# Kernel tuning notes

Hardware: AMD Instinct MI355X
Metric: run time of the kernel (lower is better)

## Reference

```python
import jax, jax.numpy as jnp
import numpy as np

HEADS = 8


def setup_inputs() -> dict:
    key = jax.random.key(0)
    ks = jax.random.split(key, 7)
    b, t, e, h = 4, 2048, 128, HEADS
    x = jax.random.normal(ks[0], (b, t, e), dtype=jnp.float32)
    mask = jax.random.randint(ks[1], (1, t, t), 0, 2, dtype=jnp.int32)
    Wq = jax.random.normal(ks[2], (e, e * h), dtype=jnp.float32) / np.sqrt(e)
    Wk = jax.random.normal(ks[3], (e, e * h), dtype=jnp.float32) / np.sqrt(e)
    Wv = jax.random.normal(ks[4], (e, e * h), dtype=jnp.float32) / np.sqrt(e)
    Wu = jax.random.normal(ks[5], (e * h, e), dtype=jnp.float32) / np.sqrt(e * h)
    bu = jax.random.normal(ks[6], (e,), dtype=jnp.float32) * 0.01
    return {"x": x, "mask": mask, "Wq": Wq, "Wk": Wk, "Wv": Wv, "Wu": Wu, "bu": bu}


def reference(x, mask, Wq, Wk, Wv, Wu, bu):
    b, t, e = x.shape
    h = HEADS
    scale = e ** (-0.25)  # original scales q and k each by e**(1/4)
    # project and split heads: (b, t, h, e) -> (b, h, t, e)
    q = (x @ Wq).reshape(b, t, h, e).transpose(0, 2, 1, 3) * scale
    k = (x @ Wk).reshape(b, t, h, e).transpose(0, 2, 1, 3) * scale
    v = (x @ Wv).reshape(b, t, h, e).transpose(0, 2, 1, 3)
    dot = jnp.einsum('bhqe,bhke->bhqk', q, k)  # (b, h, t, t)
    # causal mask: strictly-upper triangle set to -inf (mask_diagonal=False -> offset=1)
    causal = jnp.triu(jnp.ones((t, t), dtype=bool), k=1)
    dot = jnp.where(causal, jnp.float32(-np.inf), dot)
    # external mask: positions where mask == 0 set to -1e9 (broadcast over b*h)
    dot = jnp.where((mask == 0)[:, None, :, :], jnp.float32(-1e9), dot)
    att = jax.nn.softmax(dot, axis=-1)
    out = jnp.einsum('bhqk,bhke->bhqe', att, v)
    out = out.transpose(0, 2, 1, 3).reshape(b, t, h * e)
    return out @ Wu + bu
```

## Files before the change

### kernel.cpp

```cpp
#include <hip/hip_runtime.h>
#include <hip/hip_bf16.h>

typedef unsigned short u16;
typedef unsigned int u32;
typedef __attribute__((ext_vector_type(8))) short bf16x8;
typedef __attribute__((ext_vector_type(4))) float f32x4;
typedef __attribute__((ext_vector_type(8))) unsigned short u16x8;
typedef __attribute__((ext_vector_type(2))) unsigned int u32x2;

#define T_ 2048
#define H_ 8
#define BH_ 32
#define M_ 8192
#define SCALE_QK 0.29730177875068026f
#define LOG2E 1.4426950408889634f

__device__ __forceinline__ u16 f2bf(float f) {
  union { __hip_bfloat16 h; u16 u; } cv; cv.h = __float2bfloat16(f); return cv.u;
}
__device__ __forceinline__ float bf2f(u16 u) {
  union { u16 u; __hip_bfloat16 h; } cv; cv.u = u; return __bfloat162float(cv.h);
}


__global__ __launch_bounds__(256)
void prep_kernel(const float* __restrict__ x, const float* __restrict__ Wq,
                 const float* __restrict__ Wk, const float* __restrict__ Wv,
                 const float* __restrict__ Wu,
                 u16* __restrict__ xb, u16* __restrict__ WT, u16* __restrict__ WuT)
{
  int i = blockIdx.x * 256 + threadIdx.x;
  if (i < M_ * 128) { xb[i] = f2bf(x[i]); return; }
  int j = i - M_ * 128;
  if (j < 3072 * 128) {
    int n = j >> 7, k = j & 127;
    float w;
    if (n < 1024)      w = Wq[k * 1024 + n] * (SCALE_QK * LOG2E);
    else if (n < 2048) w = Wk[k * 1024 + (n - 1024)] * SCALE_QK;
    else               w = Wv[k * 1024 + (n - 2048)];
    WT[j] = f2bf(w);
    return;
  }
  int u = j - 3072 * 128;
  if (u < 128 * 1024) {
    int n = u >> 10, k = u & 1023;
    WuT[u] = f2bf(Wu[k * 128 + n]);
  }
}

__global__ __launch_bounds__(256)
void maskprep_kernel(const int* __restrict__ mask, u32* __restrict__ mbits,
                     u32* __restrict__ deglist, u32* __restrict__ degcount,
                     float* __restrict__ cnt0inv)
{
  int wave = threadIdx.x >> 6, lane = threadIdx.x & 63;
  int q = blockIdx.x * 4 + wave;
  const int* row = mask + (long)q * 2048;
  unsigned long long anyvis = 0ull;
  int cnt1 = 0;
  for (int it = 0; it < 32; ++it) {
    int k = it * 64 + lane;
    unsigned long long bal = __ballot(row[k] != 0);
    if (lane == 0) {
      mbits[q * 64 + it * 2]     = (u32)bal;
      mbits[q * 64 + it * 2 + 1] = (u32)(bal >> 32);
    }
    cnt1 += __popcll(bal);
    int lim = q - it * 64;
    if (lim >= 63)      anyvis |= bal;
    else if (lim >= 0)  anyvis |= (bal & ((2ull << lim) - 1ull));
  }
  if (lane == 0) {
    int c0 = 2048 - cnt1;
    cnt0inv[q] = (c0 > 0) ? 1.0f / (float)c0 : 0.0f;
    if (anyvis == 0ull) {
      u32 slot = atomicAdd(degcount, 1u);
      deglist[slot] = (u32)q;
    }
  }
}

__global__ __launch_bounds__(256)
void qkv_kernel(const u16* __restrict__ xb, const u16* __restrict__ WT,
                u16* __restrict__ Qb, u16* __restrict__ Kimg, u16* __restrict__ Vimg)
{
  __shared__ __align__(16) u16 As[128 * 128];
  __shared__ __align__(16) u16 Bs[128 * 128];
  const int tid = threadIdx.x;
  const int n0 = blockIdx.x * 128;
  const int m0 = blockIdx.y * 128;
#pragma unroll
  for (int i = 0; i < 8; ++i) {
    int c = tid + 256 * i;
    int row = c >> 4, d0 = (c & 15) * 8;
    int soff = row * 128 + ((((d0 >> 3)) ^ (row & 15)) << 3);
    *(u16x8*)(&As[soff]) = *(const u16x8*)(&xb[(m0 + row) * 128 + d0]);
    *(u16x8*)(&Bs[soff]) = *(const u16x8*)(&WT[(n0 + row) * 128 + d0]);
  }
  __syncthreads();
  const int wave = tid >> 6, lane = tid & 63;
  const int lr = lane & 15, lg = lane >> 4;
  const int wm = (wave >> 1) * 64, wn = (wave & 1) * 64;
  f32x4 acc[4][4];
#pragma unroll
  for (int a = 0; a < 4; ++a)
#pragma unroll
    for (int b = 0; b < 4; ++b) acc[a][b] = (f32x4){0.f, 0.f, 0.f, 0.f};
#pragma unroll
  for (int ks = 0; ks < 4; ++ks) {
    bf16x8 af[4], bf[4];
#pragma unroll
    for (int mt = 0; mt < 4; ++mt) {
      int row = wm + mt * 16 + lr, chunk = lg + ks * 4;
      af[mt] = *(const bf16x8*)(&As[row * 128 + ((chunk ^ (row & 15)) << 3)]);
    }
#pragma unroll
    for (int nt = 0; nt < 4; ++nt) {
      int row = wn + nt * 16 + lr, chunk = lg + ks * 4;
      bf[nt] = *(const bf16x8*)(&Bs[row * 128 + ((chunk ^ (row & 15)) << 3)]);
    }
#pragma unroll
    for (int mt = 0; mt < 4; ++mt)
#pragma unroll
      for (int nt = 0; nt < 4; ++nt)
        acc[mt][nt] = __builtin_amdgcn_mfma_f32_16x16x32_bf16(af[mt], bf[nt], acc[mt][nt], 0, 0, 0);
  }
  const int mat = n0 >> 10;
  const int hh = (n0 & 1023) >> 7;
  const int bb = m0 >> 11;
  const long bhb = (long)(bb * H_ + hh);
  __syncthreads();
  if (mat != 2) {
#pragma unroll
    for (int mt = 0; mt < 4; ++mt)
#pragma unroll
      for (int nt = 0; nt < 4; ++nt)
#pragma unroll
        for (int r = 0; r < 4; ++r) {
          int tl = wm + mt * 16 + lg * 4 + r;
          int d  = wn + nt * 16 + lr;
          As[tl * 128 + ((((d >> 3)) ^ (tl & 15)) << 3) + (d & 7)] = f2bf(acc[mt][nt][r]);
        }
    __syncthreads();
    if (mat == 0) {
#pragma unroll
      for (int i = 0; i < 8; ++i) {
        int c = tid + 256 * i;
        int row = c >> 4, d0 = (c & 15) * 8;
        u16x8 v = *(const u16x8*)(&As[row * 128 + ((((d0 >> 3)) ^ (row & 15)) << 3)]);
        *(u16x8*)(&Qb[(bhb * T_ + ((m0 + row) & 2047)) * 128 + d0]) = v;
      }
    } else {
#pragma unroll
      for (int i = 0; i < 8; ++i) {
        int c = tid + 256 * i;
        int row = c >> 4, d0 = (c & 15) * 8;
        u16x8 v = *(const u16x8*)(&As[row * 128 + ((((d0 >> 3)) ^ (row & 15)) << 3)]);
        int t = (m0 + row) & 2047;
        int kt = t >> 6, kr = t & 63;
        *(u16x8*)(&Kimg[(bhb * 32 + kt) * 8192 + kr * 128 + ((((d0 >> 3)) ^ (kr & 15)) << 3)]) = v;
      }
    }
  } else {
    u16* TT = As;
#pragma unroll
    for (int mt = 0; mt < 4; ++mt)
#pragma unroll
      for (int nt = 0; nt < 4; ++nt)
#pragma unroll
        for (int r = 0; r < 4; ++r) {
          int tl = wm + mt * 16 + lg * 4 + r;
          int d  = wn + nt * 16 + lr;
          TT[d * 128 + ((((tl >> 3)) ^ (d & 15)) << 3) + (tl & 7)] = f2bf(acc[mt][nt][r]);
        }
    __syncthreads();
    const int tg0 = m0 & 2047;
#pragma unroll
    for (int i = 0; i < 8; ++i) {
      int c = tid + 256 * i;
      int d = c >> 4, t0 = (c & 15) * 8;
      u16x8 v = *(const u16x8*)(&TT[d * 128 + ((((t0 >> 3)) ^ (d & 15)) << 3)]);
      int tg = tg0 + t0;
      int kt = tg >> 6, kk = tg & 63;
      *(u16x8*)(&Vimg[(bhb * 32 + kt) * 8192 + d * 64 + (((kk >> 3) ^ (d & 7)) << 3)]) = v;
    }
  }
}

__global__ __launch_bounds__(256, 3)
void flash_kernel(const u16* __restrict__ Qb, const u16* __restrict__ Kimg,
                  const u16* __restrict__ Vimg, const u32* __restrict__ mbits,
                  u16* __restrict__ Ob)
{
  __shared__ __align__(16) u16 Ks[64 * 128];
  __shared__ __align__(16) u16 VTs[128 * 64];
  __shared__ __align__(16) u16 Ps[4][16 * 64];
  const int tid = threadIdx.x;
  const int g = blockIdx.x >> 5;
  const int a_ = g & 7, quad = g >> 3;
  const int qt = (quad == 0) ? (31 - a_) : (quad == 1) ? (8 + a_)
               : (quad == 2) ? (23 - a_) : a_;
  const int bh = blockIdx.x & 31;
  const int q0 = qt * 64;
  const int wave = tid >> 6, lane = tid & 63;
  const int lr = lane & 15, lg = lane >> 4;
  const long base = (long)bh * T_ * 128;
  const long iblk = (long)bh * 32;
  const int ldsoff = wave * 2048 + lane * 8;
  const int qrl = wave * 16 + lr;
  const int swz = (lr & 7) << 1;

  bf16x8 qf[4];
  {
    const u16* qrow = Qb + base + (long)(q0 + qrl) * 128;
#pragma unroll
    for (int ks = 0; ks < 4; ++ks)
      qf[ks] = *(const bf16x8*)(&qrow[lg * 8 + ks * 32]);
  }
  f32x4 acc[8];
#pragma unroll
  for (int i = 0; i < 8; ++i) acc[i] = (f32x4){0.f, 0.f, 0.f, 0.f};
  float mrun = -__builtin_inff(), lrun = 0.f;

  u16x8 kreg[4], vreg[4];
  {
    const u16* ks0 = Kimg + iblk * 8192 + ldsoff;
    const u16* vs0 = Vimg + iblk * 8192 + ldsoff;
#pragma unroll
    for (int i = 0; i < 4; ++i) {
      kreg[i] = *(const u16x8*)(ks0 + i * 512);
      vreg[i] = *(const u16x8*)(vs0 + i * 512);
    }
  }

  for (int kt = 0; kt <= qt; ++kt) {
    __syncthreads();
#pragma unroll
    for (int i = 0; i < 4; ++i) {
      *(u16x8*)(&Ks[ldsoff + i * 512]) = kreg[i];
      *(u16x8*)(&VTs[ldsoff + i * 512]) = vreg[i];
    }
    __syncthreads();
    if (kt < qt) {
      const u16* ksn = Kimg + (iblk + kt + 1) * 8192 + ldsoff;
      const u16* vsn = Vimg + (iblk + kt + 1) * 8192 + ldsoff;
#pragma unroll
      for (int i = 0; i < 4; ++i) {
        kreg[i] = *(const u16x8*)(ksn + i * 512);
        vreg[i] = *(const u16x8*)(vsn + i * 512);
      }
    }
    u32 mw0, mw1;
    {
      const u32* mp = &mbits[(q0 + qrl) * 64 + kt * 2];
      mw0 = mp[0]; mw1 = mp[1];
    }

    f32x4 s[4];
    __builtin_amdgcn_s_setprio(1);
#pragma unroll
    for (int ft = 0; ft < 4; ++ft) {
      f32x4 sa = (f32x4){0.f, 0.f, 0.f, 0.f};
#pragma unroll
      for (int ks = 0; ks < 4; ++ks) {
        int kr = ft * 16 + lr, chunk = lg + ks * 4;
        bf16x8 kf = *(const bf16x8*)(&Ks[kr * 128 + ((chunk ^ (kr & 15)) << 3)]);
        sa = __builtin_amdgcn_mfma_f32_16x16x32_bf16(kf, qf[ks], sa, 0, 0, 0);
      }
      s[ft] = sa;
    }
    __builtin_amdgcn_s_setprio(0);
    const bool diag = (kt == qt);
#pragma unroll
    for (int ft = 0; ft < 4; ++ft) {
      u32 w = (ft & 2) ? mw1 : mw0;
      int kbase = ft * 16 + lg * 4;
      int sh = ((ft & 1) << 4) + lg * 4;
#pragma unroll
      for (int r = 0; r < 4; ++r) {
        bool vis = (w >> (sh + r)) & 1u;
        if (diag && (kbase + r) > qrl) vis = false;
        if (!vis) s[ft][r] = -__builtin_inff();
      }
    }
    float t0 = fmaxf(fmaxf(s[0][0], s[0][1]), fmaxf(s[0][2], s[0][3]));
    float t1 = fmaxf(fmaxf(s[1][0], s[1][1]), fmaxf(s[1][2], s[1][3]));
    float t2 = fmaxf(fmaxf(s[2][0], s[2][1]), fmaxf(s[2][2], s[2][3]));
    float t3 = fmaxf(fmaxf(s[3][0], s[3][1]), fmaxf(s[3][2], s[3][3]));
    float tm = fmaxf(fmaxf(t0, t1), fmaxf(t2, t3));
    tm = fmaxf(tm, __shfl_xor(tm, 16));
    tm = fmaxf(tm, __shfl_xor(tm, 32));
    float mnew = fmaxf(mrun, tm);
    float msafe = (mnew == -__builtin_inff()) ? 0.f : mnew;
    float fac = __builtin_amdgcn_exp2f(mrun - msafe);
    const bool grew = (mnew != mrun);
    mrun = mnew;
    float rs = 0.f;
#pragma unroll
    for (int ft = 0; ft < 4; ++ft) {
      float p0 = __builtin_amdgcn_exp2f(s[ft][0] - msafe);
      float p1 = __builtin_amdgcn_exp2f(s[ft][1] - msafe);
      float p2 = __builtin_amdgcn_exp2f(s[ft][2] - msafe);
      float p3 = __builtin_amdgcn_exp2f(s[ft][3] - msafe);
      s[ft][0] = p0; s[ft][1] = p1; s[ft][2] = p2; s[ft][3] = p3;
      rs += (p0 + p1) + (p2 + p3);
    }
    rs += __shfl_xor(rs, 16);
    rs += __shfl_xor(rs, 32);
    lrun = lrun * fac + rs;
    if (__any(grew)) {
#pragma unroll
      for (int nt = 0; nt < 8; ++nt)
#pragma unroll
        for (int r = 0; r < 4; ++r) acc[nt][r] *= fac;
    }
#pragma unroll
    for (int ft = 0; ft < 4; ++ft) {
      u16 h0 = f2bf(s[ft][0]), h1 = f2bf(s[ft][1]);
      u16 h2 = f2bf(s[ft][2]), h3 = f2bf(s[ft][3]);
      u32x2 pw; pw[0] = (u32)h0 | ((u32)h1 << 16); pw[1] = (u32)h2 | ((u32)h3 << 16);
      int ch4 = (ft * 4 + lg) ^ swz;
      *(u32x2*)(&Ps[wave][lr * 64 + ch4 * 4]) = pw;
    }
    bf16x8 pa[2];
#pragma unroll
    for (int s2 = 0; s2 < 2; ++s2) {
      int ch4b = (s2 * 8 + lg * 2) ^ swz;
      pa[s2] = *(const bf16x8*)(&Ps[wave][lr * 64 + ch4b * 4]);
    }
    __builtin_amdgcn_s_setprio(1);
#pragma unroll
    for (int nt = 0; nt < 8; ++nt)
#pragma unroll
      for (int s2 = 0; s2 < 2; ++s2) {
        int d = nt * 16 + lr, chunk = lg + s2 * 4;
        bf16x8 vf = *(const bf16x8*)(&VTs[d * 64 + ((chunk ^ (d & 7)) << 3)]);
        acc[nt] = __builtin_amdgcn_mfma_f32_16x16x32_bf16(vf, pa[s2], acc[nt], 0, 0, 0);
      }
    __builtin_amdgcn_s_setprio(0);
  }
  const float inv = (lrun > 0.f) ? 1.f / lrun : 0.f;
  const long orow = base + (long)(q0 + qrl) * 128;
#pragma unroll
  for (int nt = 0; nt < 8; ++nt) {
    u16 h0 = f2bf(acc[nt][0] * inv), h1 = f2bf(acc[nt][1] * inv);
    u16 h2 = f2bf(acc[nt][2] * inv), h3 = f2bf(acc[nt][3] * inv);
    u32x2 ow; ow[0] = (u32)h0 | ((u32)h1 << 16); ow[1] = (u32)h2 | ((u32)h3 << 16);
    *(u32x2*)(&Ob[orow + nt * 16 + lg * 4]) = ow;
  }
}

__global__ __launch_bounds__(256)
void fixup_partial_kernel(const u32* __restrict__ deglist, const u32* __restrict__ degcount,
                          const u32* __restrict__ mbits, const u16* __restrict__ Vimg,
                          float* __restrict__ partial)
{
  const int slot = blockIdx.z;
  const u32 cnt = *degcount;
  if (slot >= (int)cnt) return;
  const int ksec = blockIdx.x, bh = blockIdx.y;
  const int q = (int)deglist[slot];
  const int t = threadIdx.x;
  const int d = t & 127, kc = t >> 7;
  const u16* vb = Vimg + ((long)bh * 32 + ksec) * 8192 + d * 64;
  const u32 w0 = mbits[q * 64 + ksec * 2];
  const u32 w1 = mbits[q * 64 + ksec * 2 + 1];
  float a = 0.f;
#pragma unroll
  for (int i = 0; i < 4; ++i) {
    int c = kc * 4 + i;
    u32 bits = ((kc == 0) ? (w0 >> (c * 8)) : (w1 >> ((c - 4) * 8))) & 0xffu;
    u16x8 v = *(const u16x8*)(&vb[(c ^ (d & 7)) << 3]);
#pragma unroll
    for (int j = 0; j < 8; ++j)
      a += ((bits >> j) & 1u) ? 0.f : bf2f(v[j]);
  }
  __shared__ float tmp[2][128];
  tmp[kc][d] = a;
  __syncthreads();
  if (t < 128)
    partial[(((long)slot * BH_ + bh) * 128 + d) * 32 + ksec] = tmp[0][d] + tmp[1][d];
}

__global__ __launch_bounds__(128)
void fixup_combine_kernel(const u32* __restrict__ deglist, const u32* __restrict__ degcount,
                          const float* __restrict__ cnt0inv, const float* __restrict__ partial,
                          u16* __restrict__ Ob)
{
  const int slot = blockIdx.x;
  const u32 cnt = *degcount;
  if (slot >= (int)cnt) return;
  const int bh = blockIdx.y;
  const int q = (int)deglist[slot];
  const int d = threadIdx.x;
  const float* p = partial + (((long)slot * BH_ + bh) * 128 + d) * 32;
  float s = 0.f;
#pragma unroll
  for (int i = 0; i < 8; ++i) {
    f32x4 v = *(const f32x4*)(&p[i * 4]);
    s += (v[0] + v[1]) + (v[2] + v[3]);
  }
  Ob[((long)bh * T_ + q) * 128 + d] = f2bf(s * cnt0inv[q]);
}

__global__ __launch_bounds__(256)
void fixup_slow_kernel(const u32* __restrict__ deglist, const u32* __restrict__ degcount,
                       const float* __restrict__ cnt0inv, const u32* __restrict__ mbits,
                       const u16* __restrict__ Vimg, u16* __restrict__ Ob)
{
  const u32 cnt = *degcount;
  const int bh = blockIdx.y;
  const int d = threadIdx.x & 127, half = threadIdx.x >> 7;
  __shared__ float tmp[2][128];
  const u16* vb = Vimg + (long)bh * 32 * 8192;
  for (u32 idx = 8 + blockIdx.x; idx < cnt; idx += gridDim.x) {
    const int q = (int)deglist[idx];
    const float inv = cnt0inv[q];
    float a = 0.f;
#pragma unroll 16
    for (int i = 0; i < 128; ++i) {
      int k0 = half * 1024 + i * 8;
      u32 w = mbits[q * 64 + (k0 >> 5)];
      u32 bits = (w >> (k0 & 31)) & 0xffu;
      int kt = k0 >> 6, kk = k0 & 63;
      u16x8 v = *(const u16x8*)(&vb[(long)kt * 8192 + d * 64 + (((kk >> 3) ^ (d & 7)) << 3)]);
#pragma unroll
      for (int j = 0; j < 8; ++j)
        a += ((bits >> j) & 1u) ? 0.f : bf2f(v[j]);
    }
    tmp[half][d] = a;
    __syncthreads();
    if (half == 0)
      Ob[((long)bh * T_ + q) * 128 + d] = f2bf((tmp[0][d] + tmp[1][d]) * inv);
    __syncthreads();
  }
}

__global__ __launch_bounds__(256)
void outproj_kernel(const u16* __restrict__ Ob, const u16* __restrict__ WuT,
                    const float* __restrict__ bu, float* __restrict__ out)
{
  __shared__ __align__(16) u16 As[32 * 128];
  __shared__ __align__(16) u16 Bs[128 * 128];
  const int tid = threadIdx.x;
  const int m0 = blockIdx.x * 32;
  const int wave = tid >> 6, lane = tid & 63;
  const int lr = lane & 15, lg = lane >> 4;
  f32x4 acc[2][2];
#pragma unroll
  for (int a = 0; a < 2; ++a)
#pragma unroll
    for (int b = 0; b < 2; ++b) acc[a][b] = (f32x4){0.f, 0.f, 0.f, 0.f};
  for (int kc = 0; kc < 8; ++kc) {
    __syncthreads();
#pragma unroll
    for (int i = 0; i < 2; ++i) {
      int c = tid + 256 * i;
      int row = c >> 4, d0 = (c & 15) * 8;
      int m = m0 + row, bb = m >> 11, t = m & 2047;
      *(u16x8*)(&As[row * 128 + ((((d0 >> 3)) ^ (row & 15)) << 3)]) =
          *(const u16x8*)(&Ob[((long)(bb * H_ + kc) * T_ + t) * 128 + d0]);
    }
#pragma unroll
    for (int i = 0; i < 8; ++i) {
      int c = tid + 256 * i;
      int row = c >> 4, d0 = (c & 15) * 8;
      *(u16x8*)(&Bs[row * 128 + ((((d0 >> 3)) ^ (row & 15)) << 3)]) =
          *(const u16x8*)(&WuT[row * 1024 + kc * 128 + d0]);
    }
    __syncthreads();
#pragma unroll
    for (int ks = 0; ks < 4; ++ks) {
      bf16x8 af[2], bf2[2];
#pragma unroll
      for (int mt = 0; mt < 2; ++mt) {
        int row = mt * 16 + lr, chunk = lg + ks * 4;
        af[mt] = *(const bf16x8*)(&As[row * 128 + ((chunk ^ (row & 15)) << 3)]);
      }
#pragma unroll
      for (int nt = 0; nt < 2; ++nt) {
        int row = wave * 32 + nt * 16 + lr, chunk = lg + ks * 4;
        bf2[nt] = *(const bf16x8*)(&Bs[row * 128 + ((chunk ^ (row & 15)) << 3)]);
      }
#pragma unroll
      for (int mt = 0; mt < 2; ++mt)
#pragma unroll
        for (int nt = 0; nt < 2; ++nt)
          acc[mt][nt] = __builtin_amdgcn_mfma_f32_16x16x32_bf16(af[mt], bf2[nt], acc[mt][nt], 0, 0, 0);
    }
  }
#pragma unroll
  for (int mt = 0; mt < 2; ++mt)
#pragma unroll
    for (int nt = 0; nt < 2; ++nt) {
      int n = wave * 32 + nt * 16 + lr;
      float bias = bu[n];
#pragma unroll
      for (int r = 0; r < 4; ++r) {
        int m = m0 + mt * 16 + lg * 4 + r;
        out[(long)m * 128 + n] = acc[mt][nt][r] + bias;
      }
    }
}

extern "C" void kernel_launch(void* const* d_in, const int* in_sizes, int n_in,
                              void* d_out, int out_size, void* d_ws, size_t ws_size,
                              hipStream_t stream)
{
  (void)in_sizes; (void)n_in; (void)out_size; (void)ws_size;
  const float* x   = (const float*)d_in[0];
  const int*   msk = (const int*)d_in[1];
  const float* Wq  = (const float*)d_in[2];
  const float* Wk  = (const float*)d_in[3];
  const float* Wv  = (const float*)d_in[4];
  const float* Wu  = (const float*)d_in[5];
  const float* bu  = (const float*)d_in[6];
  float* out = (float*)d_out;

  u16* Qb   = (u16*)d_ws;
  u16* Kimg = Qb + (size_t)BH_ * T_ * 128;
  u16* Vimg = Kimg + (size_t)BH_ * T_ * 128;
  u16* Obf  = Vimg + (size_t)BH_ * T_ * 128;
  u16* xb   = Obf + (size_t)BH_ * T_ * 128;
  u16* WT   = xb + (size_t)M_ * 128;
  u16* WuT  = WT + (size_t)3072 * 128;
  u32* mbits   = (u32*)(WuT + (size_t)128 * 1024);
  u32* deglist = mbits + (size_t)2048 * 64;
  u32* degcount = deglist + 2048;
  float* cnt0inv = (float*)(degcount + 1);
  float* partial = (float*)Qb;

  hipMemsetAsync(degcount, 0, sizeof(u32), stream);
  prep_kernel<<<6144, 256, 0, stream>>>(x, Wq, Wk, Wv, Wu, xb, WT, WuT);
  maskprep_kernel<<<512, 256, 0, stream>>>(msk, mbits, deglist, degcount, cnt0inv);
  qkv_kernel<<<dim3(24, 64), 256, 0, stream>>>(xb, WT, Qb, Kimg, Vimg);
  flash_kernel<<<1024, 256, 0, stream>>>(Qb, Kimg, Vimg, mbits, Obf);
  fixup_partial_kernel<<<dim3(32, 32, 8), 256, 0, stream>>>(deglist, degcount, mbits, Vimg, partial);
  fixup_combine_kernel<<<dim3(8, 32), 128, 0, stream>>>(deglist, degcount, cnt0inv, partial, Obf);
  fixup_slow_kernel<<<dim3(32, 32), 256, 0, stream>>>(deglist, degcount, cnt0inv, mbits, Vimg, Obf);
  outproj_kernel<<<256, 256, 0, stream>>>(Obf, WuT, bu, out);
}
```

Measured before the change: 134.1 us.

## Load V fragments directly from global memory and add lazy softmax rescaling

Drops the V tile from shared memory. Each wave now loads its V MFMA operands straight from the pre-swizzled global V image into registers, split into two halves so the loads overlap with the softmax and QK work. This removes V LDS writes and reads and shrinks LDS usage, which could raise occupancy. It also adds a lazy rescale that skips updating the running max and rescaling the accumulator when no lane's max grows by more than 8 (log2 units). This trades extra global/L2 traffic, since every wave re-reads V, and more register pressure for less LDS traffic and less rescaling work.

```diff
diff --git a/kernel.cpp b/kernel.cpp
--- a/kernel.cpp
+++ b/kernel.cpp
@@ -193,7 +193,6 @@
                   u16* __restrict__ Ob)
 {
   __shared__ __align__(16) u16 Ks[64 * 128];
-  __shared__ __align__(16) u16 VTs[128 * 64];
   __shared__ __align__(16) u16 Ps[4][16 * 64];
   const int tid = threadIdx.x;
   const int g = blockIdx.x >> 5;
@@ -222,34 +221,40 @@
   for (int i = 0; i < 8; ++i) acc[i] = (f32x4){0.f, 0.f, 0.f, 0.f};
   float mrun = -__builtin_inff(), lrun = 0.f;
 
-  u16x8 kreg[4], vreg[4];
+  int voff[8][2];
+#pragma unroll
+  for (int nt = 0; nt < 8; ++nt)
+#pragma unroll
+    for (int s2 = 0; s2 < 2; ++s2) {
+      int d = nt * 16 + lr, chunk = lg + s2 * 4;
+      voff[nt][s2] = d * 64 + ((chunk ^ (d & 7)) << 3);
+    }
+
+  u16x8 kreg[4];
   {
     const u16* ks0 = Kimg + iblk * 8192 + ldsoff;
-    const u16* vs0 = Vimg + iblk * 8192 + ldsoff;
-#pragma unroll
-    for (int i = 0; i < 4; ++i) {
-      kreg[i] = *(const u16x8*)(ks0 + i * 512);
-      vreg[i] = *(const u16x8*)(vs0 + i * 512);
-    }
+#pragma unroll
+    for (int i = 0; i < 4; ++i) kreg[i] = *(const u16x8*)(ks0 + i * 512);
   }
 
   for (int kt = 0; kt <= qt; ++kt) {
     __syncthreads();
 #pragma unroll
-    for (int i = 0; i < 4; ++i) {
+    for (int i = 0; i < 4; ++i)
       *(u16x8*)(&Ks[ldsoff + i * 512]) = kreg[i];
-      *(u16x8*)(&VTs[ldsoff + i * 512]) = vreg[i];
-    }
     __syncthreads();
     if (kt < qt) {
       const u16* ksn = Kimg + (iblk + kt + 1) * 8192 + ldsoff;
-      const u16* vsn = Vimg + (iblk + kt + 1) * 8192 + ldsoff;
-#pragma unroll
-      for (int i = 0; i < 4; ++i) {
-        kreg[i] = *(const u16x8*)(ksn + i * 512);
-        vreg[i] = *(const u16x8*)(vsn + i * 512);
-      }
-    }
+#pragma unroll
+      for (int i = 0; i < 4; ++i) kreg[i] = *(const u16x8*)(ksn + i * 512);
+    }
+    const u16* vblk = Vimg + (iblk + kt) * 8192;
+    bf16x8 vfA[4][2];
+#pragma unroll
+    for (int nt = 0; nt < 4; ++nt)
+#pragma unroll
+      for (int s2 = 0; s2 < 2; ++s2)
+        vfA[nt][s2] = *(const bf16x8*)(&vblk[voff[nt][s2]]);
     u32 mw0, mw1;
     {
       const u32* mp = &mbits[(q0 + qrl) * 64 + kt * 2];
@@ -290,11 +295,15 @@
     float tm = fmaxf(fmaxf(t0, t1), fmaxf(t2, t3));
     tm = fmaxf(tm, __shfl_xor(tm, 16));
     tm = fmaxf(tm, __shfl_xor(tm, 32));
-    float mnew = fmaxf(mrun, tm);
-    float msafe = (mnew == -__builtin_inff()) ? 0.f : mnew;
-    float fac = __builtin_amdgcn_exp2f(mrun - msafe);
-    const bool grew = (mnew != mrun);
-    mrun = mnew;
+    const bool skip = __all(tm - mrun <= 8.0f);
+    float fac = 1.0f;
+    float msafe = (mrun == -__builtin_inff()) ? 0.f : mrun;
+    if (!skip) {
+      float mnew = fmaxf(mrun, tm);
+      msafe = (mnew == -__builtin_inff()) ? 0.f : mnew;
+      fac = __builtin_amdgcn_exp2f(mrun - msafe);
+      mrun = mnew;
+    }
     float rs = 0.f;
 #pragma unroll
     for (int ft = 0; ft < 4; ++ft) {
@@ -308,12 +317,18 @@
     rs += __shfl_xor(rs, 16);
     rs += __shfl_xor(rs, 32);
     lrun = lrun * fac + rs;
-    if (__any(grew)) {
+    if (!skip) {
 #pragma unroll
       for (int nt = 0; nt < 8; ++nt)
 #pragma unroll
         for (int r = 0; r < 4; ++r) acc[nt][r] *= fac;
     }
+    bf16x8 vfB[4][2];
+#pragma unroll
+    for (int nt = 0; nt < 4; ++nt)
+#pragma unroll
+      for (int s2 = 0; s2 < 2; ++s2)
+        vfB[nt][s2] = *(const bf16x8*)(&vblk[voff[nt + 4][s2]]);
 #pragma unroll
     for (int ft = 0; ft < 4; ++ft) {
       u16 h0 = f2bf(s[ft][0]), h1 = f2bf(s[ft][1]);
@@ -330,13 +345,15 @@
     }
     __builtin_amdgcn_s_setprio(1);
 #pragma unroll
-    for (int nt = 0; nt < 8; ++nt)
-#pragma unroll
-      for (int s2 = 0; s2 < 2; ++s2) {
-        int d = nt * 16 + lr, chunk = lg + s2 * 4;
-        bf16x8 vf = *(const bf16x8*)(&VTs[d * 64 + ((chunk ^ (d & 7)) << 3)]);
-        acc[nt] = __builtin_amdgcn_mfma_f32_16x16x32_bf16(vf, pa[s2], acc[nt], 0, 0, 0);
-      }
+    for (int nt = 0; nt < 4; ++nt)
+#pragma unroll
+      for (int s2 = 0; s2 < 2; ++s2)
+        acc[nt] = __builtin_amdgcn_mfma_f32_16x16x32_bf16(vfA[nt][s2], pa[s2], acc[nt], 0, 0, 0);
+#pragma unroll
+    for (int nt = 0; nt < 4; ++nt)
+#pragma unroll
+      for (int s2 = 0; s2 < 2; ++s2)
+        acc[nt + 4] = __builtin_amdgcn_mfma_f32_16x16x32_bf16(vfB[nt][s2], pa[s2], acc[nt + 4], 0, 0, 0);
     __builtin_amdgcn_s_setprio(0);
   }
   const float inv = (lrun > 0.f) ? 1.f / lrun : 0.f;
```

Result: slower. 247.9 us, median of 4 (+84.8%).
